# Performance work log

Measured on AMD Instinct MI355X. Metric: run time of the kernel, lower is better.

## Reference

```python
import jax, jax.numpy as jnp
import numpy as np

BN_EPS = 1e-5
N_NODES = 100000
N_EDGES = 800000


def setup_inputs() -> dict:
    key = jax.random.key(0)
    ks = jax.random.split(key, 8)
    d = {
        "v": jax.random.normal(ks[0], (N_NODES, 86), dtype=jnp.float32),
        "edges": jax.random.randint(ks[1], (2, N_EDGES), 0, N_NODES, dtype=jnp.int64),
        # encoder (3 Linear+ReLU layers)
        "We1": jax.random.normal(ks[2], (86, 128), dtype=jnp.float32) * 0.1,
        "be1": jnp.zeros((128,), jnp.float32),
        "We2": jax.random.normal(ks[3], (128, 256), dtype=jnp.float32) * 0.1,
        "be2": jnp.zeros((256,), jnp.float32),
        "We3": jax.random.normal(ks[4], (256, 512), dtype=jnp.float32) * 0.1,
        "be3": jnp.zeros((512,), jnp.float32),
        # GIN layers: eps (train_eps, init 0), Linear W/b, BatchNorm gamma/beta
        "eps1": jnp.float32(0.0),
        "W1": jax.random.normal(ks[5], (86, 128), dtype=jnp.float32) * 0.1,
        "b1": jnp.zeros((128,), jnp.float32),
        "g1": jnp.ones((128,), jnp.float32),
        "bt1": jnp.zeros((128,), jnp.float32),
        "eps2": jnp.float32(0.0),
        "W2": jax.random.normal(ks[6], (128, 256), dtype=jnp.float32) * 0.1,
        "b2": jnp.zeros((256,), jnp.float32),
        "g2": jnp.ones((256,), jnp.float32),
        "bt2": jnp.zeros((256,), jnp.float32),
        "eps3": jnp.float32(0.0),
        "W3": jax.random.normal(ks[7], (256, 512), dtype=jnp.float32) * 0.1,
        "b3": jnp.zeros((512,), jnp.float32),
        "g3": jnp.ones((512,), jnp.float32),
        "bt3": jnp.zeros((512,), jnp.float32),
    }
    return d


def _bn(x, g, b):
    # BatchNorm1d in training mode: batch (node-dim) stats, biased variance
    m = x.mean(axis=0)
    var = x.var(axis=0)
    return (x - m) * jax.lax.rsqrt(var + BN_EPS) * g + b


def _gin(x, src, dst, n, eps, W, b, g, beta):
    # GINConv: nn((1+eps)*x_i + sum_{j in N(i)} x_j), then Linear-BN-ReLU
    agg = jax.ops.segment_sum(x[src], dst, num_segments=n)
    h = (1.0 + eps) * x + agg
    return jax.nn.relu(_bn(h @ W + b, g, beta))


def reference(v, edges, We1, be1, We2, be2, We3, be3,
              eps1, W1, b1, g1, bt1,
              eps2, W2, b2, g2, bt2,
              eps3, W3, b3, g3, bt3):
    src, dst = edges[0], edges[1]
    n = v.shape[0]
    # encoder hidden states
    v1 = jax.nn.relu(v @ We1 + be1)
    v2 = jax.nn.relu(v1 @ We2 + be2)
    v3 = jax.nn.relu(v2 @ We3 + be3)
    # GIN stack with residual adds from encoder
    x1 = _gin(v, src, dst, n, eps1, W1, b1, g1, bt1)
    xv1 = x1 + v1
    x2 = _gin(xv1, src, dst, n, eps2, W2, b2, g2, bt2)
    xv2 = x2 + v2
    x3 = _gin(xv2, src, dst, n, eps3, W3, b3, g3, bt3)
    return x3 + v3
```

## Files before the change

kernel.cpp:

```cpp
#include <hip/hip_runtime.h>


typedef short short8 __attribute__((ext_vector_type(8)));
typedef float f32x4 __attribute__((ext_vector_type(4)));

__device__ __forceinline__ unsigned short f2bf(float f) {
    unsigned int u = __float_as_uint(f);
    u = (u + 0x7fffu + ((u >> 16) & 1u)) >> 16;
    return (unsigned short)u;
}
__device__ __forceinline__ float bflo(unsigned int u) { return __uint_as_float(u << 16); }
__device__ __forceinline__ float bfhi(unsigned int u) { return __uint_as_float(u & 0xffff0000u); }
__device__ __forceinline__ unsigned int packbf2(float lo, float hi) {
    return (unsigned int)f2bf(lo) | ((unsigned int)f2bf(hi) << 16);
}
__device__ __forceinline__ float bf2f(unsigned short s) {
    return __uint_as_float(((unsigned int)s) << 16);
}

__device__ __forceinline__ void gload16(const void* g, void* l) {
    __builtin_amdgcn_global_load_lds(
        (__attribute__((address_space(1))) const unsigned int*)g,
        (__attribute__((address_space(3))) unsigned int*)l, 16, 0, 0);
}


__global__ void count_deg_kernel(const int* __restrict__ dst, int E, int* __restrict__ deg) {
    int e = blockIdx.x * blockDim.x + threadIdx.x;
    if (e < E) atomicAdd(&deg[dst[e]], 1);
}

__global__ __launch_bounds__(256)
void scan_reduce_kernel(const int* __restrict__ deg, int M, int* __restrict__ bsum) {
    __shared__ int ws[4];
    int t = threadIdx.x;
    int i0 = blockIdx.x * 1024 + t * 4;
    int s = 0;
    if (i0 + 3 < M) {
        int4 v = *(const int4*)(deg + i0);
        s = v.x + v.y + v.z + v.w;
    } else {
        for (int i = i0; i < min(i0 + 4, M); ++i) s += deg[i];
    }
    for (int d = 1; d < 64; d <<= 1) s += __shfl_xor(s, d);
    if ((t & 63) == 0) ws[t >> 6] = s;
    __syncthreads();
    if (t == 0) bsum[blockIdx.x] = ws[0] + ws[1] + ws[2] + ws[3];
}

__global__ __launch_bounds__(1024)
void scan_bsum_kernel(const int* __restrict__ bsum, int NB,
                      int* __restrict__ boff, int* __restrict__ off, int M) {
    __shared__ int lds[1024];
    int t = threadIdx.x;
    int v = (t < NB) ? bsum[t] : 0;
    lds[t] = v;
    __syncthreads();
    for (int d = 1; d < 1024; d <<= 1) {
        int x = (t >= d) ? lds[t - d] : 0;
        __syncthreads();
        lds[t] += x;
        __syncthreads();
    }
    if (t < NB) boff[t] = lds[t] - v;
    if (t == NB - 1) off[M] = lds[t];
}

__global__ __launch_bounds__(256)
void scan_apply_kernel(const int* __restrict__ deg, int M, const int* __restrict__ boff,
                       int* __restrict__ off, int* __restrict__ cur) {
    __shared__ int lds[256];
    int t = threadIdx.x;
    int i0 = blockIdx.x * 1024 + t * 4;
    int d0 = 0, d1 = 0, d2 = 0, d3 = 0;
    if (i0 + 3 < M) {
        int4 v = *(const int4*)(deg + i0);
        d0 = v.x; d1 = v.y; d2 = v.z; d3 = v.w;
    } else {
        if (i0 + 0 < M) d0 = deg[i0 + 0];
        if (i0 + 1 < M) d1 = deg[i0 + 1];
        if (i0 + 2 < M) d2 = deg[i0 + 2];
        if (i0 + 3 < M) d3 = deg[i0 + 3];
    }
    int s = d0 + d1 + d2 + d3;
    lds[t] = s;
    __syncthreads();
    for (int d = 1; d < 256; d <<= 1) {
        int x = (t >= d) ? lds[t - d] : 0;
        __syncthreads();
        lds[t] += x;
        __syncthreads();
    }
    int e = lds[t] - s + boff[blockIdx.x];
    int e0 = e, e1 = e + d0, e2 = e1 + d1, e3 = e2 + d2;
    if (i0 + 3 < M) {
        *(int4*)(off + i0) = make_int4(e0, e1, e2, e3);
        *(int4*)(cur + i0) = make_int4(e0, e1, e2, e3);
    } else {
        if (i0 + 0 < M) { off[i0 + 0] = e0; cur[i0 + 0] = e0; }
        if (i0 + 1 < M) { off[i0 + 1] = e1; cur[i0 + 1] = e1; }
        if (i0 + 2 < M) { off[i0 + 2] = e2; cur[i0 + 2] = e2; }
        if (i0 + 3 < M) { off[i0 + 3] = e3; cur[i0 + 3] = e3; }
    }
}

__global__ void fill_kernel(const int* __restrict__ src, const int* __restrict__ dst, int E,
                            int* __restrict__ cur, int* __restrict__ srcs) {
    int e = blockIdx.x * blockDim.x + threadIdx.x;
    if (e < E) {
        int p = atomicAdd(&cur[dst[e]], 1);
        srcs[p] = src[e];
    }
}

template <int D>
__global__ __launch_bounds__(256)
void gather_h_kernel(const unsigned short* __restrict__ x, const int* __restrict__ off,
                     const int* __restrict__ srcs, const float* __restrict__ epsp,
                     unsigned short* __restrict__ h, int M) {
    constexpr int C = D / 128;
    int lane = threadIdx.x & 63;
    int node = blockIdx.x * 4 + (threadIdx.x >> 6);
    if (node >= M) return;
    float accx[C], accy[C];
#pragma unroll
    for (int c = 0; c < C; ++c) { accx[c] = 0.f; accy[c] = 0.f; }
    int j0 = off[node], j1 = off[node + 1];
    for (int j = j0; j < j1; ++j) {
        const unsigned int* row = (const unsigned int*)(x + (size_t)srcs[j] * D);
#pragma unroll
        for (int c = 0; c < C; ++c) {
            unsigned int u = row[lane + c * 64];
            accx[c] += bflo(u);
            accy[c] += bfhi(u);
        }
    }
    float e = 1.0f + epsp[0];
    const unsigned int* self = (const unsigned int*)(x + (size_t)node * D);
    unsigned int* out = (unsigned int*)(h + (size_t)node * D);
#pragma unroll
    for (int c = 0; c < C; ++c) {
        unsigned int u = self[lane + c * 64];
        float lo = __builtin_fmaf(e, bflo(u), accx[c]);
        float hi = __builtin_fmaf(e, bfhi(u), accy[c]);
        out[lane + c * 64] = packbf2(lo, hi);
    }
}


__global__ void prep_wt_kernel(const float* __restrict__ W, unsigned short* __restrict__ WT,
                               int K, int N, int Kp) {
    int id = blockIdx.x * 256 + threadIdx.x;
    if (id >= N * Kp) return;
    int n = id / Kp, k = id - n * Kp;
    float v = (k < K) ? W[(size_t)k * N + n] : 0.f;
    WT[id] = f2bf(v);
}

__global__ void conv_v_kernel(const float* __restrict__ v, unsigned short* __restrict__ vbf, int M) {
    int id = blockIdx.x * 256 + threadIdx.x;
    if (id >= M * 128) return;
    int r = id >> 7, k = id & 127;
    float x = (k < 86) ? v[(size_t)r * 86 + k] : 0.f;
    vbf[id] = f2bf(x);
}

__global__ void finalize_kernel(const float* __restrict__ s1, const float* __restrict__ s2,
                                const float* __restrict__ g, const float* __restrict__ bt,
                                int M, int N, float* __restrict__ scale, float* __restrict__ shift) {
    int c = blockIdx.x * 128 + threadIdx.x;
    if (c >= N) return;
    float inv = 1.0f / (float)M;
    float mean = s1[c] * inv;
    float var = s2[c] * inv - mean * mean;
    float sc = g[c] * rsqrtf(var + 1e-5f);
    scale[c] = sc;
    shift[c] = __builtin_fmaf(-mean, sc, bt[c]);
}

template <int Kp, int N, int MODE>
__global__ __launch_bounds__(256, 2)
void mfma_gemm(const unsigned short* __restrict__ A, const unsigned short* __restrict__ WT,
               const float* __restrict__ bias,
               const unsigned short* __restrict__ Y, const float* __restrict__ scale,
               const float* __restrict__ shift,
               float* __restrict__ s1g, float* __restrict__ s2g,
               void* __restrict__ out0, unsigned short* __restrict__ out_v, int M) {
    constexpr int BK = 64;
    __shared__ unsigned short lA[128 * BK];
    __shared__ unsigned short lB[128 * BK];
    const int t = threadIdx.x;
    const int l = t & 63, w = t >> 6;
    const int wr = w >> 1, wc = w & 1;
    const int bm = blockIdx.y * 128, bn = blockIdx.x * 128;
    const int ln = l & 15, lg = l >> 4;

    f32x4 acc[4][4] = {};

    const int srow0 = w * 32;
    const int srow = srow0 + (l >> 3);
    const int sc8 = l & 7;

    for (int k0 = 0; k0 < Kp; k0 += BK) {
#pragma unroll
        for (int i = 0; i < 4; ++i) {
            int row = srow + i * 8;
            int gc = sc8 ^ (row & 7);
            int gra = bm + row;
            gra = gra < M ? gra : M - 1;
            gload16(A + (size_t)gra * Kp + k0 + gc * 8, &lA[(srow0 + i * 8) * BK]);
            gload16(WT + (size_t)(bn + row) * Kp + k0 + gc * 8, &lB[(srow0 + i * 8) * BK]);
        }
        __syncthreads();
#pragma unroll
        for (int ks = 0; ks < 2; ++ks) {
            short8 af[4], bfr[4];
#pragma unroll
            for (int m = 0; m < 4; ++m) {
                int row = wr * 64 + m * 16 + ln;
                int g = ks * 4 + lg;
                af[m] = *(const short8*)&lA[row * BK + ((g ^ (row & 7)) * 8)];
            }
#pragma unroll
            for (int n = 0; n < 4; ++n) {
                int row = wc * 64 + n * 16 + ln;
                int g = ks * 4 + lg;
                bfr[n] = *(const short8*)&lB[row * BK + ((g ^ (row & 7)) * 8)];
            }
#pragma unroll
            for (int m = 0; m < 4; ++m)
#pragma unroll
                for (int n = 0; n < 4; ++n)
                    acc[m][n] = __builtin_amdgcn_mfma_f32_16x16x32_bf16(af[m], bfr[n], acc[m][n], 0, 0, 0);
        }
        __syncthreads();
    }

    const int col0 = bn + wc * 64 + ln;
    float bj[4];
#pragma unroll
    for (int n = 0; n < 4; ++n) bj[n] = bias[col0 + n * 16];

    if constexpr (MODE == 0) {
        unsigned short* outp = (unsigned short*)out0;
        float s1l[4] = {0.f, 0.f, 0.f, 0.f}, s2l[4] = {0.f, 0.f, 0.f, 0.f};
#pragma unroll
        for (int m = 0; m < 4; ++m) {
#pragma unroll
            for (int r = 0; r < 4; ++r) {
                int row = bm + wr * 64 + m * 16 + lg * 4 + r;
                if (row < M) {
                    size_t base = (size_t)row * N;
#pragma unroll
                    for (int n = 0; n < 4; ++n) {
                        float y = acc[m][n][r] + bj[n];
                        outp[base + col0 + n * 16] = f2bf(y);
                        s1l[n] += y;
                        s2l[n] = __builtin_fmaf(y, y, s2l[n]);
                    }
                }
            }
        }
#pragma unroll
        for (int n = 0; n < 4; ++n) {
            s1l[n] += __shfl_xor(s1l[n], 16);
            s1l[n] += __shfl_xor(s1l[n], 32);
            s2l[n] += __shfl_xor(s2l[n], 16);
            s2l[n] += __shfl_xor(s2l[n], 32);
        }
        __syncthreads();
        float* red = (float*)lA;
        if (lg == 0) {
#pragma unroll
            for (int n = 0; n < 4; ++n) {
                int cidx = wc * 64 + n * 16 + ln;
                red[wr * 256 + cidx] = s1l[n];
                red[wr * 256 + 128 + cidx] = s2l[n];
            }
        }
        __syncthreads();
        if (t < 128) {
            atomicAdd(&s1g[bn + t], red[t] + red[256 + t]);
            atomicAdd(&s2g[bn + t], red[128 + t] + red[384 + t]);
        }
    } else {
        float scl[4], shf[4];
#pragma unroll
        for (int n = 0; n < 4; ++n) {
            scl[n] = scale[col0 + n * 16];
            shf[n] = shift[col0 + n * 16];
        }
#pragma unroll
        for (int m = 0; m < 4; ++m) {
#pragma unroll
            for (int r = 0; r < 4; ++r) {
                int row = bm + wr * 64 + m * 16 + lg * 4 + r;
                if (row >= M) continue;
                size_t base = (size_t)row * N;
#pragma unroll
                for (int n = 0; n < 4; ++n) {
                    size_t idx = base + col0 + n * 16;
                    float enc = fmaxf(acc[m][n][r] + bj[n], 0.f);
                    float yv = bf2f(Y[idx]);
                    float o = enc + fmaxf(__builtin_fmaf(yv, scl[n], shf[n]), 0.f);
                    if constexpr (MODE == 1) {
                        out_v[idx] = f2bf(enc);
                        ((unsigned short*)out0)[idx] = f2bf(o);
                    } else {
                        ((float*)out0)[idx] = o;
                    }
                }
            }
        }
    }
}


extern "C" void kernel_launch(void* const* d_in, const int* in_sizes, int n_in,
                              void* d_out, int out_size, void* d_ws, size_t ws_size,
                              hipStream_t stream) {
    const float* v   = (const float*)d_in[0];
    const int*   edg = (const int*)d_in[1];
    const float* We1 = (const float*)d_in[2];  const float* be1 = (const float*)d_in[3];
    const float* We2 = (const float*)d_in[4];  const float* be2 = (const float*)d_in[5];
    const float* We3 = (const float*)d_in[6];  const float* be3 = (const float*)d_in[7];
    const float* eps1 = (const float*)d_in[8];
    const float* W1 = (const float*)d_in[9];   const float* b1 = (const float*)d_in[10];
    const float* g1 = (const float*)d_in[11];  const float* bt1 = (const float*)d_in[12];
    const float* eps2 = (const float*)d_in[13];
    const float* W2 = (const float*)d_in[14];  const float* b2 = (const float*)d_in[15];
    const float* g2 = (const float*)d_in[16];  const float* bt2 = (const float*)d_in[17];
    const float* eps3 = (const float*)d_in[18];
    const float* W3 = (const float*)d_in[19];  const float* b3 = (const float*)d_in[20];
    const float* g3 = (const float*)d_in[21];  const float* bt3 = (const float*)d_in[22];

    const int M = in_sizes[0] / 86;
    const int E = in_sizes[1] / 2;
    const int* src = edg;
    const int* dst = edg + E;

    char* w = (char*)d_ws;
    auto carve = [&](size_t bytes) -> void* {
        void* p = (void*)w;
        w += (bytes + 255) & ~(size_t)255;
        return p;
    };
    int*   deg  = (int*)carve((size_t)M * 4);
    int*   off  = (int*)carve((size_t)(M + 1) * 4);
    int*   cur  = (int*)carve((size_t)M * 4);
    int*   srcs = (int*)carve((size_t)E * 4);
    int*   bsum = (int*)carve(1024 * 4);
    int*   boff = (int*)carve(1024 * 4);
    unsigned short* vbf = (unsigned short*)carve((size_t)M * 128 * 2);
    unsigned short* hb  = (unsigned short*)carve((size_t)M * 256 * 2);
    unsigned short* yb  = (unsigned short*)carve((size_t)M * 512 * 2);
    unsigned short* v1  = (unsigned short*)carve((size_t)M * 128 * 2);
    unsigned short* v2  = (unsigned short*)carve((size_t)M * 256 * 2);
    unsigned short* xv1 = (unsigned short*)carve((size_t)M * 128 * 2);
    unsigned short* xv2 = (unsigned short*)carve((size_t)M * 256 * 2);
    unsigned short* WT1g = (unsigned short*)carve(128 * 128 * 2);
    unsigned short* WT1e = (unsigned short*)carve(128 * 128 * 2);
    unsigned short* WT2g = (unsigned short*)carve(256 * 128 * 2);
    unsigned short* WT2e = (unsigned short*)carve(256 * 128 * 2);
    unsigned short* WT3g = (unsigned short*)carve(512 * 256 * 2);
    unsigned short* WT3e = (unsigned short*)carve(512 * 256 * 2);
    float* stats = (float*)carve(3 * 2048 * 4);

    hipMemsetAsync(deg, 0, (size_t)M * 4, stream);
    hipMemsetAsync(stats, 0, 3 * 2048 * 4, stream);

    conv_v_kernel<<<(M * 128 + 255) / 256, 256, 0, stream>>>(v, vbf, M);
    prep_wt_kernel<<<(128 * 128 + 255) / 256, 256, 0, stream>>>(W1, WT1g, 86, 128, 128);
    prep_wt_kernel<<<(128 * 128 + 255) / 256, 256, 0, stream>>>(We1, WT1e, 86, 128, 128);
    prep_wt_kernel<<<(256 * 128 + 255) / 256, 256, 0, stream>>>(W2, WT2g, 128, 256, 128);
    prep_wt_kernel<<<(256 * 128 + 255) / 256, 256, 0, stream>>>(We2, WT2e, 128, 256, 128);
    prep_wt_kernel<<<(512 * 256 + 255) / 256, 256, 0, stream>>>(W3, WT3g, 256, 512, 256);
    prep_wt_kernel<<<(512 * 256 + 255) / 256, 256, 0, stream>>>(We3, WT3e, 256, 512, 256);

    const int NB = (M + 1023) / 1024;
    count_deg_kernel<<<(E + 255) / 256, 256, 0, stream>>>(dst, E, deg);
    scan_reduce_kernel<<<NB, 256, 0, stream>>>(deg, M, bsum);
    scan_bsum_kernel<<<1, 1024, 0, stream>>>(bsum, NB, boff, off, M);
    scan_apply_kernel<<<NB, 256, 0, stream>>>(deg, M, boff, off, cur);
    fill_kernel<<<(E + 255) / 256, 256, 0, stream>>>(src, dst, E, cur, srcs);

    const int MB = (M + 127) / 128;
    float* st;

    st = stats + 0 * 2048;
    gather_h_kernel<128><<<(M + 3) / 4, 256, 0, stream>>>(vbf, off, srcs, eps1, hb, M);
    mfma_gemm<128, 128, 0><<<dim3(1, MB), 256, 0, stream>>>(
        hb, WT1g, b1, nullptr, nullptr, nullptr, st, st + 512, yb, nullptr, M);
    finalize_kernel<<<1, 128, 0, stream>>>(st, st + 512, g1, bt1, M, 128, st + 1024, st + 1536);
    mfma_gemm<128, 128, 1><<<dim3(1, MB), 256, 0, stream>>>(
        vbf, WT1e, be1, yb, st + 1024, st + 1536, nullptr, nullptr, xv1, v1, M);

    st = stats + 1 * 2048;
    gather_h_kernel<128><<<(M + 3) / 4, 256, 0, stream>>>(xv1, off, srcs, eps2, hb, M);
    mfma_gemm<128, 256, 0><<<dim3(2, MB), 256, 0, stream>>>(
        hb, WT2g, b2, nullptr, nullptr, nullptr, st, st + 512, yb, nullptr, M);
    finalize_kernel<<<2, 128, 0, stream>>>(st, st + 512, g2, bt2, M, 256, st + 1024, st + 1536);
    mfma_gemm<128, 256, 1><<<dim3(2, MB), 256, 0, stream>>>(
        v1, WT2e, be2, yb, st + 1024, st + 1536, nullptr, nullptr, xv2, v2, M);

    st = stats + 2 * 2048;
    gather_h_kernel<256><<<(M + 3) / 4, 256, 0, stream>>>(xv2, off, srcs, eps3, hb, M);
    mfma_gemm<256, 512, 0><<<dim3(4, MB), 256, 0, stream>>>(
        hb, WT3g, b3, nullptr, nullptr, nullptr, st, st + 512, yb, nullptr, M);
    finalize_kernel<<<4, 128, 0, stream>>>(st, st + 512, g3, bt3, M, 512, st + 1024, st + 1536);
    mfma_gemm<256, 512, 2><<<dim3(4, MB), 256, 0, stream>>>(
        v2, WT3e, be3, yb, st + 1024, st + 1536, nullptr, nullptr, (float*)d_out, nullptr, M);
}
```

Measured before the change: 915.8 us.

## Fuse prep kernels, fold BN finalize into GEMM, split and unroll gather

Merges the input conversion and six weight-transpose kernels into one launch. Moves the BatchNorm finalize step into the prologue of the second GEMM, so three finalize launches go away. The neighbour gather now unrolls by four edges for more loads in flight, and the 256-wide layer splits each node across two waves. The final fp32 output uses nontemporal stores. Together these cut launch overhead and raise memory-level parallelism in the gather, at the cost of each GEMM block recomputing scale and shift redundantly.

```diff
diff --git a/kernel.cpp b/kernel.cpp
--- a/kernel.cpp
+++ b/kernel.cpp
@@ -113,78 +113,86 @@
     }
 }
 
-template <int D>
+template <int WPN>
 __global__ __launch_bounds__(256)
 void gather_h_kernel(const unsigned short* __restrict__ x, const int* __restrict__ off,
                      const int* __restrict__ srcs, const float* __restrict__ epsp,
                      unsigned short* __restrict__ h, int M) {
-    constexpr int C = D / 128;
+    constexpr int RU = WPN * 64;
     int lane = threadIdx.x & 63;
-    int node = blockIdx.x * 4 + (threadIdx.x >> 6);
+    int gw = blockIdx.x * 4 + (threadIdx.x >> 6);
+    int node = (WPN == 1) ? gw : (gw >> 1);
+    int chunk = (WPN == 1) ? 0 : (gw & 1);
     if (node >= M) return;
-    float accx[C], accy[C];
-#pragma unroll
-    for (int c = 0; c < C; ++c) { accx[c] = 0.f; accy[c] = 0.f; }
+    const unsigned int* xc = (const unsigned int*)x + chunk * 64 + lane;
+    float ax = 0.f, ay = 0.f;
     int j0 = off[node], j1 = off[node + 1];
-    for (int j = j0; j < j1; ++j) {
-        const unsigned int* row = (const unsigned int*)(x + (size_t)srcs[j] * D);
-#pragma unroll
-        for (int c = 0; c < C; ++c) {
-            unsigned int u = row[lane + c * 64];
-            accx[c] += bflo(u);
-            accy[c] += bfhi(u);
-        }
+    int j = j0;
+    for (; j + 3 < j1; j += 4) {
+        int s0 = srcs[j + 0], s1 = srcs[j + 1], s2 = srcs[j + 2], s3 = srcs[j + 3];
+        unsigned int u0 = xc[(size_t)s0 * RU];
+        unsigned int u1 = xc[(size_t)s1 * RU];
+        unsigned int u2 = xc[(size_t)s2 * RU];
+        unsigned int u3 = xc[(size_t)s3 * RU];
+        ax += bflo(u0); ay += bfhi(u0);
+        ax += bflo(u1); ay += bfhi(u1);
+        ax += bflo(u2); ay += bfhi(u2);
+        ax += bflo(u3); ay += bfhi(u3);
+    }
+    for (; j < j1; ++j) {
+        unsigned int u = xc[(size_t)srcs[j] * RU];
+        ax += bflo(u); ay += bfhi(u);
     }
     float e = 1.0f + epsp[0];
-    const unsigned int* self = (const unsigned int*)(x + (size_t)node * D);
-    unsigned int* out = (unsigned int*)(h + (size_t)node * D);
-#pragma unroll
-    for (int c = 0; c < C; ++c) {
-        unsigned int u = self[lane + c * 64];
-        float lo = __builtin_fmaf(e, bflo(u), accx[c]);
-        float hi = __builtin_fmaf(e, bfhi(u), accy[c]);
-        out[lane + c * 64] = packbf2(lo, hi);
-    }
-}
-
-
-__global__ void prep_wt_kernel(const float* __restrict__ W, unsigned short* __restrict__ WT,
-                               int K, int N, int Kp) {
-    int id = blockIdx.x * 256 + threadIdx.x;
-    if (id >= N * Kp) return;
-    int n = id / Kp, k = id - n * Kp;
+    unsigned int su = xc[(size_t)node * RU];
+    ((unsigned int*)h)[(size_t)node * RU + chunk * 64 + lane] =
+        packbf2(__builtin_fmaf(e, bflo(su), ax), __builtin_fmaf(e, bfhi(su), ay));
+}
+
+__device__ __forceinline__ void wt_fill(const float* __restrict__ W, unsigned short* __restrict__ WT,
+                                        int id, int K, int N, int KpShift) {
+    int n = id >> KpShift, k = id & ((1 << KpShift) - 1);
     float v = (k < K) ? W[(size_t)k * N + n] : 0.f;
     WT[id] = f2bf(v);
 }
 
-__global__ void conv_v_kernel(const float* __restrict__ v, unsigned short* __restrict__ vbf, int M) {
+__global__ void prep_all_kernel(const float* __restrict__ v, unsigned short* __restrict__ vbf,
+                                const float* __restrict__ W1, const float* __restrict__ We1,
+                                unsigned short* __restrict__ WT1g, unsigned short* __restrict__ WT1e,
+                                const float* __restrict__ W2, const float* __restrict__ We2,
+                                unsigned short* __restrict__ WT2g, unsigned short* __restrict__ WT2e,
+                                const float* __restrict__ W3, const float* __restrict__ We3,
+                                unsigned short* __restrict__ WT3g, unsigned short* __restrict__ WT3e,
+                                int M) {
     int id = blockIdx.x * 256 + threadIdx.x;
-    if (id >= M * 128) return;
-    int r = id >> 7, k = id & 127;
-    float x = (k < 86) ? v[(size_t)r * 86 + k] : 0.f;
-    vbf[id] = f2bf(x);
-}
-
-__global__ void finalize_kernel(const float* __restrict__ s1, const float* __restrict__ s2,
-                                const float* __restrict__ g, const float* __restrict__ bt,
-                                int M, int N, float* __restrict__ scale, float* __restrict__ shift) {
-    int c = blockIdx.x * 128 + threadIdx.x;
-    if (c >= N) return;
-    float inv = 1.0f / (float)M;
-    float mean = s1[c] * inv;
-    float var = s2[c] * inv - mean * mean;
-    float sc = g[c] * rsqrtf(var + 1e-5f);
-    scale[c] = sc;
-    shift[c] = __builtin_fmaf(-mean, sc, bt[c]);
+    int nv = M * 128;
+    if (id < nv) {
+        int r = id >> 7, k = id & 127;
+        float x = (k < 86) ? v[(size_t)r * 86 + k] : 0.f;
+        vbf[id] = f2bf(x);
+        return;
+    }
+    id -= nv;
+    if (id < 16384) { wt_fill(W1, WT1g, id, 86, 128, 7); return; }
+    id -= 16384;
+    if (id < 16384) { wt_fill(We1, WT1e, id, 86, 128, 7); return; }
+    id -= 16384;
+    if (id < 32768) { wt_fill(W2, WT2g, id, 128, 256, 7); return; }
+    id -= 32768;
+    if (id < 32768) { wt_fill(We2, WT2e, id, 128, 256, 7); return; }
+    id -= 32768;
+    if (id < 131072) { wt_fill(W3, WT3g, id, 256, 512, 8); return; }
+    id -= 131072;
+    if (id < 131072) { wt_fill(We3, WT3e, id, 256, 512, 8); return; }
 }
 
 template <int Kp, int N, int MODE>
 __global__ __launch_bounds__(256, 2)
 void mfma_gemm(const unsigned short* __restrict__ A, const unsigned short* __restrict__ WT,
                const float* __restrict__ bias,
-               const unsigned short* __restrict__ Y, const float* __restrict__ scale,
-               const float* __restrict__ shift,
+               const unsigned short* __restrict__ Y,
                float* __restrict__ s1g, float* __restrict__ s2g,
+               const float* __restrict__ gam, const float* __restrict__ bet,
                void* __restrict__ out0, unsigned short* __restrict__ out_v, int M) {
     constexpr int BK = 64;
     __shared__ unsigned short lA[128 * BK];
@@ -197,6 +205,21 @@
 
     f32x4 acc[4][4] = {};
 
+    const int col0 = bn + wc * 64 + ln;
+    float scl[4], shf[4];
+    if constexpr (MODE != 0) {
+        float inv = 1.0f / (float)M;
+#pragma unroll
+        for (int n = 0; n < 4; ++n) {
+            int c = col0 + n * 16;
+            float mean = s1g[c] * inv;
+            float var = s2g[c] * inv - mean * mean;
+            float sc = gam[c] * rsqrtf(var + 1e-5f);
+            scl[n] = sc;
+            shf[n] = __builtin_fmaf(-mean, sc, bet[c]);
+        }
+    }
+
     const int srow0 = w * 32;
     const int srow = srow0 + (l >> 3);
     const int sc8 = l & 7;
@@ -236,7 +259,6 @@
         __syncthreads();
     }
 
-    const int col0 = bn + wc * 64 + ln;
     float bj[4];
 #pragma unroll
     for (int n = 0; n < 4; ++n) bj[n] = bias[col0 + n * 16];
@@ -284,12 +306,6 @@
             atomicAdd(&s2g[bn + t], red[128 + t] + red[384 + t]);
         }
     } else {
-        float scl[4], shf[4];
-#pragma unroll
-        for (int n = 0; n < 4; ++n) {
-            scl[n] = scale[col0 + n * 16];
-            shf[n] = shift[col0 + n * 16];
-        }
 #pragma unroll
         for (int m = 0; m < 4; ++m) {
 #pragma unroll
@@ -307,7 +323,7 @@
                         out_v[idx] = f2bf(enc);
                         ((unsigned short*)out0)[idx] = f2bf(o);
                     } else {
-                        ((float*)out0)[idx] = o;
+                        __builtin_nontemporal_store(o, &((float*)out0)[idx]);
                     }
                 }
             }
@@ -364,18 +380,16 @@
     unsigned short* WT2e = (unsigned short*)carve(256 * 128 * 2);
     unsigned short* WT3g = (unsigned short*)carve(512 * 256 * 2);
     unsigned short* WT3e = (unsigned short*)carve(512 * 256 * 2);
-    float* stats = (float*)carve(3 * 2048 * 4);
+    float* stats = (float*)carve(3 * 1024 * 4);
 
     hipMemsetAsync(deg, 0, (size_t)M * 4, stream);
-    hipMemsetAsync(stats, 0, 3 * 2048 * 4, stream);
-
-    conv_v_kernel<<<(M * 128 + 255) / 256, 256, 0, stream>>>(v, vbf, M);
-    prep_wt_kernel<<<(128 * 128 + 255) / 256, 256, 0, stream>>>(W1, WT1g, 86, 128, 128);
-    prep_wt_kernel<<<(128 * 128 + 255) / 256, 256, 0, stream>>>(We1, WT1e, 86, 128, 128);
-    prep_wt_kernel<<<(256 * 128 + 255) / 256, 256, 0, stream>>>(W2, WT2g, 128, 256, 128);
-    prep_wt_kernel<<<(256 * 128 + 255) / 256, 256, 0, stream>>>(We2, WT2e, 128, 256, 128);
-    prep_wt_kernel<<<(512 * 256 + 255) / 256, 256, 0, stream>>>(W3, WT3g, 256, 512, 256);
-    prep_wt_kernel<<<(512 * 256 + 255) / 256, 256, 0, stream>>>(We3, WT3e, 256, 512, 256);
+    hipMemsetAsync(stats, 0, 3 * 1024 * 4, stream);
+
+    {
+        int total = M * 128 + 2 * (16384 + 32768 + 131072);
+        prep_all_kernel<<<(total + 255) / 256, 256, 0, stream>>>(
+            v, vbf, W1, We1, WT1g, WT1e, W2, We2, WT2g, WT2e, W3, We3, WT3g, WT3e, M);
+    }
 
     const int NB = (M + 1023) / 1024;
     count_deg_kernel<<<(E + 255) / 256, 256, 0, stream>>>(dst, E, deg);
@@ -387,27 +401,24 @@
     const int MB = (M + 127) / 128;
     float* st;
 
-    st = stats + 0 * 2048;
-    gather_h_kernel<128><<<(M + 3) / 4, 256, 0, stream>>>(vbf, off, srcs, eps1, hb, M);
+    st = stats + 0 * 1024;
+    gather_h_kernel<1><<<(M + 3) / 4, 256, 0, stream>>>(vbf, off, srcs, eps1, hb, M);
     mfma_gemm<128, 128, 0><<<dim3(1, MB), 256, 0, stream>>>(
-        hb, WT1g, b1, nullptr, nullptr, nullptr, st, st + 512, yb, nullptr, M);
-    finalize_kernel<<<1, 128, 0, stream>>>(st, st + 512, g1, bt1, M, 128, st + 1024, st + 1536);
+        hb, WT1g, b1, nullptr, st, st + 512, nullptr, nullptr, yb, nullptr, M);
     mfma_gemm<128, 128, 1><<<dim3(1, MB), 256, 0, stream>>>(
-        vbf, WT1e, be1, yb, st + 1024, st + 1536, nullptr, nullptr, xv1, v1, M);
-
-    st = stats + 1 * 2048;
-    gather_h_kernel<128><<<(M + 3) / 4, 256, 0, stream>>>(xv1, off, srcs, eps2, hb, M);
+        vbf, WT1e, be1, yb, st, st + 512, g1, bt1, xv1, v1, M);
+
+    st = stats + 1 * 1024;
+    gather_h_kernel<1><<<(M + 3) / 4, 256, 0, stream>>>(xv1, off, srcs, eps2, hb, M);
     mfma_gemm<128, 256, 0><<<dim3(2, MB), 256, 0, stream>>>(
-        hb, WT2g, b2, nullptr, nullptr, nullptr, st, st + 512, yb, nullptr, M);
-    finalize_kernel<<<2, 128, 0, stream>>>(st, st + 512, g2, bt2, M, 256, st + 1024, st + 1536);
+        hb, WT2g, b2, nullptr, st, st + 512, nullptr, nullptr, yb, nullptr, M);
     mfma_gemm<128, 256, 1><<<dim3(2, MB), 256, 0, stream>>>(
-        v1, WT2e, be2, yb, st + 1024, st + 1536, nullptr, nullptr, xv2, v2, M);
-
-    st = stats + 2 * 2048;
-    gather_h_kernel<256><<<(M + 3) / 4, 256, 0, stream>>>(xv2, off, srcs, eps3, hb, M);
+        v1, WT2e, be2, yb, st, st + 512, g2, bt2, xv2, v2, M);
+
+    st = stats + 2 * 1024;
+    gather_h_kernel<2><<<(2 * M + 3) / 4, 256, 0, stream>>>(xv2, off, srcs, eps3, hb, M);
     mfma_gemm<256, 512, 0><<<dim3(4, MB), 256, 0, stream>>>(
-        hb, WT3g, b3, nullptr, nullptr, nullptr, st, st + 512, yb, nullptr, M);
-    finalize_kernel<<<4, 128, 0, stream>>>(st, st + 512, g3, bt3, M, 512, st + 1024, st + 1536);
+        hb, WT3g, b3, nullptr, st, st + 512, nullptr, nullptr, yb, nullptr, M);
     mfma_gemm<256, 512, 2><<<dim3(4, MB), 256, 0, stream>>>(
-        v2, WT3e, be3, yb, st + 1024, st + 1536, nullptr, nullptr, (float*)d_out, nullptr, M);
-}
+        v2, WT3e, be3, yb, st, st + 512, g3, bt3, (float*)d_out, nullptr, M);
+}
```

After: 824.6 us. 10.0% less time.
